# Performance work log

Measured on AMD Instinct MI355X. Metric: run time of the kernel, lower is better.

The kernel has to match this reference:

```python
import jax, jax.numpy as jnp
import numpy as np

B, N_PER_GRAPH = 16, 512          # uniform graphs -> to_dense_batch is a reshape
N_TOKENS = B * N_PER_GRAPH
M = 32                            # neighbors per node
D_MODEL, D_EDGE, H = 256, 128, 8


def _layernorm(x, g, b, eps=1e-5):
    m = jnp.mean(x, axis=-1, keepdims=True)
    v = jnp.mean((x - m) ** 2, axis=-1, keepdims=True)
    return (x - m) * jax.lax.rsqrt(v + eps) * g + b


def _frame_ops():
    # 2^3 = 8 sign-flip operations, matches FrameAveraging.create_ops
    d = jnp.array([-1.0, 1.0], dtype=jnp.float32)
    g = jnp.meshgrid(d, d, d, indexing='ij')
    return jnp.stack(g, axis=-1).reshape(8, 3)


def _forward(token_embs, geo_feats, edge_feats, neighbor_indices, neighbor_masks,
             ln_qkv_g, ln_qkv_b, W_qkv, b_qkv, ln_e_g, ln_e_b, W_qkv_e, b_qkv_e,
             w_attn, w_edge, W_gate, b_gate, W_fc1, b_fc1, ln_h_g, ln_h_b,
             W_fc2, b_fc2, W_fa, b_fa):
    n = token_embs.shape[0]
    d_head = D_MODEL // H
    de_head = D_EDGE // H
    # qkv transformation
    qkv = _layernorm(token_embs, ln_qkv_g, ln_qkv_b) @ W_qkv + b_qkv
    q, k, v = [a.reshape(n, H, d_head) for a in jnp.split(qkv, 3, axis=-1)]
    qkve = _layernorm(edge_feats, ln_e_g, ln_e_b) @ W_qkv_e + b_qkv_e
    qe, ve = [a.reshape(n, M, H, de_head) for a in jnp.split(qkve, 2, axis=-1)]
    gate = jax.nn.sigmoid(token_embs @ W_gate + b_gate)            # [n,1]
    # GAT-style MLP attention over gathered neighbors
    message = q[:, None] + k[neighbor_indices]                     # [n,M,H,d]
    attn = jnp.einsum('nmhd,d->nmh', message, w_attn) \
         + jnp.einsum('nmhe,e->nmh', qe, w_edge)
    attn = jnp.where(neighbor_masks[..., None], attn, -1e9)
    attn = jax.nn.softmax(jnp.transpose(attn, (0, 2, 1)), axis=-1)  # [n,H,M]
    # context aggregation
    v_n = v[neighbor_indices]                                      # [n,M,H,d]
    scalar_ctx = jnp.einsum('nhm,nmhd->nhd', attn, v_n).reshape(n, -1)
    edge_ctx = jnp.einsum('nhm,nmhd->nhd', attn, ve).reshape(n, -1)
    hcat = jnp.concatenate([scalar_ctx, edge_ctx], axis=-1)
    hmid = _layernorm(jax.nn.gelu(hcat @ W_fc1 + b_fc1, approximate=False), ln_h_g, ln_h_b)
    scalar_out = hmid @ W_fc2 + b_fc2 + token_embs
    # geometric branch with frame averaging (n_heads > 1 path)
    Xb = geo_feats.reshape(B, N_PER_GRAPH, 3)                      # dense batch, full mask
    center = Xb.mean(axis=1)                                       # [B,3]
    Xc = Xb - center[:, None]
    C = jax.lax.stop_gradient(jnp.einsum('bni,bnj->bij', Xc, Xc))  # backward=False -> detach
    _, V = jnp.linalg.eigh(C)                                      # symmetric, UPLO irrelevant
    ops = _frame_ops()
    F_ops = jax.lax.stop_gradient(ops[None, :, None, :] * V[:, None])  # [B,8,3,3]
    h_fr = jnp.einsum('bpj,boji->bopi', Xc, F_ops)                 # [B,8,N,3]
    geo_f = jnp.transpose(h_fr, (1, 0, 2, 3)).reshape(8, n, 3)     # frame-major, node order b*N+p
    geo_neigh = geo_f[:, neighbor_indices]                         # [8,n,M,3]
    geo_ctx = jnp.einsum('nhm,fnmd->fnhd', attn, geo_neigh)        # [8,n,H,3]
    agg = jax.nn.silu(jnp.einsum('fnhd,h->fnd', geo_ctx, W_fa) + b_fa)  # W_frame_agg
    geo_b = jnp.transpose(agg, (1, 0, 2)).reshape(B, N_PER_GRAPH, 8, 3)
    geo_b = jnp.transpose(geo_b, (0, 2, 1, 3))                     # [B,8,N,3]
    inv = jnp.einsum('boij,bopj->bopi', F_ops, geo_b).mean(axis=1) + center[:, None]
    geo_context = inv.reshape(n, 3)
    geo_out = geo_context * gate + geo_feats * (1.0 - gate)
    return scalar_out, geo_out


def setup_inputs() -> dict:
    key = jax.random.key(0)
    ks = jax.random.split(key, 16)
    r = lambda k, shape, s=0.02: (jax.random.normal(k, shape) * s).astype(jnp.float32)
    token_embs = jax.random.normal(ks[0], (N_TOKENS, D_MODEL), dtype=jnp.float32)
    geo_feats = jax.random.normal(ks[1], (N_TOKENS, 3), dtype=jnp.float32)
    edge_feats = jax.random.normal(ks[2], (N_TOKENS, M, D_EDGE), dtype=jnp.float32)
    base = (jnp.arange(N_TOKENS) // N_PER_GRAPH) * N_PER_GRAPH
    neighbor_indices = base[:, None] + jax.random.randint(ks[3], (N_TOKENS, M), 0, N_PER_GRAPH)
    batch_idx = jnp.arange(N_TOKENS) // N_PER_GRAPH
    neighbor_masks = jax.random.uniform(ks[4], (N_TOKENS, M)) < 0.9
    d_head, de_head = D_MODEL // H, D_EDGE // H
    return dict(
        token_embs=token_embs, geo_feats=geo_feats, edge_feats=edge_feats,
        neighbor_indices=neighbor_indices, batch_idx=batch_idx, neighbor_masks=neighbor_masks,
        ln_qkv_g=jnp.ones(D_MODEL), ln_qkv_b=jnp.zeros(D_MODEL),
        W_qkv=r(ks[5], (D_MODEL, 3 * D_MODEL)), b_qkv=jnp.zeros(3 * D_MODEL),
        ln_e_g=jnp.ones(D_EDGE), ln_e_b=jnp.zeros(D_EDGE),
        W_qkv_e=r(ks[6], (D_EDGE, 2 * D_EDGE)), b_qkv_e=jnp.zeros(2 * D_EDGE),
        w_attn=r(ks[7], (d_head,), 0.1), w_edge=r(ks[8], (de_head,), 0.1),
        W_gate=jnp.zeros((D_MODEL, 1)), b_gate=jnp.ones((1,)),   # _init_params
        W_fc1=r(ks[9], (D_MODEL + D_EDGE, D_MODEL)), b_fc1=jnp.zeros(D_MODEL),
        ln_h_g=jnp.ones(D_MODEL), ln_h_b=jnp.zeros(D_MODEL),
        W_fc2=r(ks[10], (D_MODEL, D_MODEL)), b_fc2=jnp.zeros(D_MODEL),
        W_fa=r(ks[11], (H,), 0.3), b_fa=jnp.zeros((1,)),
    )


def reference(token_embs, geo_feats, edge_feats, neighbor_indices, batch_idx, neighbor_masks,
              ln_qkv_g, ln_qkv_b, W_qkv, b_qkv, ln_e_g, ln_e_b, W_qkv_e, b_qkv_e,
              w_attn, w_edge, W_gate, b_gate, W_fc1, b_fc1, ln_h_g, ln_h_b,
              W_fc2, b_fc2, W_fa, b_fa):
    # batch_idx is uniform (arange // N_PER_GRAPH); dense batching handled by reshape
    return _forward(token_embs, geo_feats, edge_feats, neighbor_indices, neighbor_masks,
                    ln_qkv_g, ln_qkv_b, W_qkv, b_qkv, ln_e_g, ln_e_b, W_qkv_e, b_qkv_e,
                    w_attn, w_edge, W_gate, b_gate, W_fc1, b_fc1, ln_h_g, ln_h_b,
                    W_fc2, b_fc2, W_fa, b_fa)
```

## Files before the change

### kernel.cpp

```cpp
#include <hip/hip_runtime.h>
#include <math.h>

#define NTOK 8192
#define NPG  512
#define MNEI 32
#define DM   256
#define DE   128
#define NH   8

#define OFF_WCAT  0u
#define OFF_BCAT  69632u
#define OFF_WEF   69904u
#define OFF_BEF   70928u
#define OFF_FLAG  70936u
#define OFF_QA    70944u
#define OFF_KA    136480u
#define OFF_GATE  202016u
#define OFF_VW    210208u
#define OFF_PROJ  2307360u
#define OFF_VMAT  2331936u
#define OFF_CEN   2332080u
#define OFF_HCAT  2332128u

#define OUT_GEO_OFF 2097152

__device__ __forceinline__ void fma16(const float* row, float w, float* acc) {
    const float4* r4 = (const float4*)row;
    float4 a0 = r4[0], a1 = r4[1], a2 = r4[2], a3 = r4[3];
    acc[0]  += a0.x*w; acc[1]  += a0.y*w; acc[2]  += a0.z*w; acc[3]  += a0.w*w;
    acc[4]  += a1.x*w; acc[5]  += a1.y*w; acc[6]  += a1.z*w; acc[7]  += a1.w*w;
    acc[8]  += a2.x*w; acc[9]  += a2.y*w; acc[10] += a2.z*w; acc[11] += a2.w*w;
    acc[12] += a3.x*w; acc[13] += a3.y*w; acc[14] += a3.z*w; acc[15] += a3.w*w;
}

__global__ __launch_bounds__(256) void k_fold(
    const float* __restrict__ Wqkv, const float* __restrict__ bqkv,
    const float* __restrict__ Wqkve, const float* __restrict__ bqkve,
    const float* __restrict__ w_attn, const float* __restrict__ w_edge,
    const int* __restrict__ maskp, float* __restrict__ ws)
{
    int t = threadIdx.x;
    if (blockIdx.x == 0) {
        __shared__ int sbad, sflt;
        if (t == 0) { sbad = 0; sflt = 0; }
        __syncthreads();
        int bad = 0, flt = 0;
        for (int i = 0; i < 256; i++) {
            unsigned int w = (unsigned int)maskp[t*256 + i];
            if (w > 1u) bad = 1;
            if (w == 0x3F800000u) flt = 1;
        }
        if (bad) atomicOr(&sbad, 1);
        if (flt) atomicOr(&sflt, 1);
        __syncthreads();
        if (t == 0) {
            int f = sflt ? 2 : (sbad ? 1 : 0);
            ((int*)(ws + OFF_FLAG))[0] = f;
        }
        return;
    }
    int gid = (blockIdx.x - 1) * 256 + t;
    if (gid < 69632) {
        int r = gid / 272, c = gid % 272;
        float val;
        if (c < 16) {
            int h = c & 7; int off = (c < 8) ? 0 : 256;
            float s = 0.f;
            for (int d = 0; d < 32; d++) s += Wqkv[r*768 + off + h*32 + d] * w_attn[d];
            val = s;
        } else {
            val = Wqkv[r*768 + 512 + (c - 16)];
        }
        ws[OFF_WCAT + gid] = val;
    } else if (gid < 69632 + 272) {
        int c = gid - 69632;
        float val;
        if (c < 16) {
            int h = c & 7; int off = (c < 8) ? 0 : 256;
            float s = 0.f;
            for (int d = 0; d < 32; d++) s += bqkv[off + h*32 + d] * w_attn[d];
            val = s;
        } else {
            val = bqkv[512 + (c - 16)];
        }
        ws[OFF_BCAT + c] = val;
    } else if (gid < 69904 + 1024) {
        int i = gid - 69904;
        int h = i >> 7, r = i & 127;
        float s = 0.f;
        for (int e = 0; e < 16; e++) s += Wqkve[r*256 + h*16 + e] * w_edge[e];
        ws[OFF_WEF + i] = s;
    } else if (gid < 70928 + 8) {
        int h = gid - 70928;
        float s = 0.f;
        for (int e = 0; e < 16; e++) s += bqkve[h*16 + e] * w_edge[e];
        ws[OFF_BEF + h] = s;
    }
}

__global__ __launch_bounds__(320) void k_tokprep(
    const float* __restrict__ tok, const float* __restrict__ ln_g,
    const float* __restrict__ ln_b, const float* __restrict__ Wgate,
    const float* __restrict__ bgate, float* __restrict__ ws)
{
    __shared__ __align__(16) float sln[256 * 20];
    int t = threadIdx.x;
    int tok0 = blockIdx.x * 16;

    for (int i = t; i < 16 * 256; i += 320) {
        int tt = i >> 8, k = i & 255;
        sln[k*20 + tt] = tok[(size_t)(tok0 + tt) * 256 + k];
    }
    __syncthreads();

    int wave = t >> 6, lane = t & 63;
    if (wave < 4) {
        for (int rr = 0; rr < 4; rr++) {
            int tt = wave * 4 + rr;
            float s = 0.f, gdot = 0.f;
            float xs[4];
            for (int i = 0; i < 4; i++) {
                int k = lane + 64 * i;
                float x = sln[k*20 + tt];
                xs[i] = x; s += x; gdot += x * Wgate[k];
            }
            for (int m = 32; m >= 1; m >>= 1) { s += __shfl_xor(s, m, 64); gdot += __shfl_xor(gdot, m, 64); }
            float mu = s * (1.0f / 256.0f);
            float vs = 0.f;
            for (int i = 0; i < 4; i++) { float d = xs[i] - mu; vs += d * d; }
            for (int m = 32; m >= 1; m >>= 1) vs += __shfl_xor(vs, m, 64);
            float rinv = rsqrtf(vs * (1.0f / 256.0f) + 1e-5f);
            for (int i = 0; i < 4; i++) {
                int k = lane + 64 * i;
                sln[k*20 + tt] = (xs[i] - mu) * rinv * ln_g[k] + ln_b[k];
            }
            if (lane == 0) ws[OFF_GATE + tok0 + tt] = 1.0f / (1.0f + expf(-(gdot + bgate[0])));
        }
    }
    __syncthreads();

    if (t < 272) {
        const float* Wc = ws + OFF_WCAT;
        float acc[16];
        #pragma unroll
        for (int i = 0; i < 16; i++) acc[i] = 0.f;
        #pragma unroll 4
        for (int k = 0; k < 256; k++) {
            float w = Wc[k*272 + t];
            fma16(&sln[k*20], w, acc);
        }
        float b = ws[OFF_BCAT + t];
        for (int tt = 0; tt < 16; tt++) {
            float val = acc[tt] + b;
            int n = tok0 + tt;
            if (t < 8)       ws[OFF_QA + n*8 + t] = val;
            else if (t < 16) ws[OFF_KA + n*8 + (t - 8)] = val;
            else             ws[OFF_VW + (size_t)n*256 + (t - 16)] = val;
        }
    }
}

__global__ __launch_bounds__(256) void k_geo(const float* __restrict__ geo, float* __restrict__ ws)
{
    __shared__ float sred[4 * 9];
    __shared__ float sres[9];
    __shared__ float sV[9];
    int t = threadIdx.x, g = blockIdx.x;
    int wave = t >> 6, lane = t & 63;
    const float* gp = geo + (size_t)g * NPG * 3;

    float x0[2], y0[2], z0[2];
    float sx = 0.f, sy = 0.f, sz = 0.f;
    for (int i = 0; i < 2; i++) {
        int p = t + 256 * i;
        x0[i] = gp[p*3 + 0]; y0[i] = gp[p*3 + 1]; z0[i] = gp[p*3 + 2];
        sx += x0[i]; sy += y0[i]; sz += z0[i];
    }
    {
        float vals[3] = {sx, sy, sz};
        for (int q = 0; q < 3; q++) {
            float v = vals[q];
            for (int m = 32; m >= 1; m >>= 1) v += __shfl_xor(v, m, 64);
            if (lane == 0) sred[wave*9 + q] = v;
        }
    }
    __syncthreads();
    if (t < 3) {
        float s = 0.f;
        for (int w = 0; w < 4; w++) s += sred[w*9 + t];
        sres[t] = s * (1.0f / 512.0f);
    }
    __syncthreads();
    float cx = sres[0], cy = sres[1], cz = sres[2];

    float c6[6] = {0.f, 0.f, 0.f, 0.f, 0.f, 0.f};
    for (int i = 0; i < 2; i++) {
        float dx = x0[i] - cx, dy = y0[i] - cy, dz = z0[i] - cz;
        c6[0] += dx*dx; c6[1] += dx*dy; c6[2] += dx*dz;
        c6[3] += dy*dy; c6[4] += dy*dz; c6[5] += dz*dz;
    }
    for (int q = 0; q < 6; q++) {
        float v = c6[q];
        for (int m = 32; m >= 1; m >>= 1) v += __shfl_xor(v, m, 64);
        if (lane == 0) sred[wave*9 + q] = v;
    }
    __syncthreads();
    if (t < 6) {
        float s = 0.f;
        for (int w = 0; w < 4; w++) s += sred[w*9 + t];
        sres[t] = s;
    }
    __syncthreads();

    if (t == 0) {
        double a[3][3];
        a[0][0] = sres[0]; a[0][1] = a[1][0] = sres[1]; a[0][2] = a[2][0] = sres[2];
        a[1][1] = sres[3]; a[1][2] = a[2][1] = sres[4]; a[2][2] = sres[5];
        double v[3][3] = {{1,0,0},{0,1,0},{0,0,1}};
        const int ps[3] = {0, 0, 1}, qs[3] = {1, 2, 2};
        for (int sweep = 0; sweep < 30; sweep++) {
            for (int pi = 0; pi < 3; pi++) {
                int p = ps[pi], q = qs[pi];
                double apq = a[p][q];
                if (fabs(apq) < 1e-300) continue;
                double theta = (a[q][q] - a[p][p]) / (2.0 * apq);
                double tt = ((theta >= 0.0) ? 1.0 : -1.0) / (fabs(theta) + sqrt(theta*theta + 1.0));
                double c = 1.0 / sqrt(tt*tt + 1.0), s = tt * c;
                int k = 3 - p - q;
                double app = a[p][p], aqq = a[q][q], akp = a[k][p], akq = a[k][q];
                a[p][p] = app - tt * apq;
                a[q][q] = aqq + tt * apq;
                a[p][q] = 0.0; a[q][p] = 0.0;
                a[k][p] = c*akp - s*akq; a[p][k] = a[k][p];
                a[k][q] = s*akp + c*akq; a[q][k] = a[k][q];
                for (int kk = 0; kk < 3; kk++) {
                    double vp = v[kk][p], vq = v[kk][q];
                    v[kk][p] = c*vp - s*vq;
                    v[kk][q] = s*vp + c*vq;
                }
            }
        }
        for (int r = 0; r < 3; r++)
            for (int c2 = 0; c2 < 3; c2++) {
                float fv = (float)v[r][c2];
                sV[r*3 + c2] = fv;
                ws[OFF_VMAT + g*9 + r*3 + c2] = fv;
            }
        ws[OFF_CEN + g*3 + 0] = cx;
        ws[OFF_CEN + g*3 + 1] = cy;
        ws[OFF_CEN + g*3 + 2] = cz;
    }
    __syncthreads();

    for (int i = 0; i < 2; i++) {
        int p = t + 256 * i;
        float dx = x0[i] - cx, dy = y0[i] - cy, dz = z0[i] - cz;
        for (int c = 0; c < 3; c++) {
            float pr = dx * sV[0*3 + c] + dy * sV[1*3 + c] + dz * sV[2*3 + c];
            ws[OFF_PROJ + (size_t)(g*NPG + p)*3 + c] = pr;
        }
    }
}

__global__ __launch_bounds__(256) void k_attn(
    const float* __restrict__ edge, const int* __restrict__ nbr,
    const void* __restrict__ maskp,
    const float* __restrict__ lneg, const float* __restrict__ lneb,
    const float* __restrict__ bqkve, const float* __restrict__ Wqkve,
    const float* __restrict__ Wfa, const float* __restrict__ bfa,
    const float* __restrict__ geo, float* __restrict__ ws, float* __restrict__ out)
{
    __shared__ __align__(16) float se[32 * 132];
    __shared__ __align__(16) float swe[8 * 132];
    __shared__ __align__(16) float sew[8 * 132];
    __shared__ float slog[264];
    __shared__ float sattn[264];
    __shared__ int   snbr[32];
    __shared__ int   smask[32];
    __shared__ float swm[32];
    __shared__ float sqa[8], sbef[8];
    __shared__ float sge[128], sbe[128];
    __shared__ float sg3[3];

    int t = threadIdx.x;
    int n = blockIdx.x;
    int g = n >> 9;
    int flag = ((const int*)(ws + OFF_FLAG))[0];

    if (t < 32) {
        snbr[t] = nbr[n*32 + t];
        int mv;
        if (flag == 1)      mv = (int)((const unsigned char*)maskp)[n*32 + t];
        else if (flag == 2) mv = (((const float*)maskp)[n*32 + t] != 0.0f) ? 1 : 0;
        else                mv = ((const int*)maskp)[n*32 + t];
        smask[t] = mv;
    }
    if (t < 8) { sqa[t] = ws[OFF_QA + n*8 + t]; sbef[t] = ws[OFF_BEF + t]; }
    if (t >= 32 && t < 160) { sge[t - 32] = lneg[t - 32]; sbe[t - 32] = lneb[t - 32]; }
    {
        const float* wef = ws + OFF_WEF;
        for (int i = 0; i < 4; i++) {
            int idx = t*4 + i;
            int h = idx >> 7, r = idx & 127;
            swe[h*132 + r] = wef[idx];
        }
    }
    {
        const float4* ep = (const float4*)(edge + (size_t)n * 4096);
        for (int j = 0; j < 4; j++) {
            int l = j*1024 + t*4;
            float4 v4 = ep[l >> 2];
            int m = l >> 7, r = l & 127;
            *(float4*)&se[m*132 + r] = v4;
        }
    }
    __syncthreads();

    {
        int m = t >> 3, sub = t & 7;
        int base = m*132 + sub*16;
        float4 x0 = *(float4*)&se[base + 0];
        float4 x1 = *(float4*)&se[base + 4];
        float4 x2 = *(float4*)&se[base + 8];
        float4 x3 = *(float4*)&se[base + 12];
        float s = x0.x+x0.y+x0.z+x0.w + x1.x+x1.y+x1.z+x1.w
                + x2.x+x2.y+x2.z+x2.w + x3.x+x3.y+x3.z+x3.w;
        for (int mm = 4; mm >= 1; mm >>= 1) s += __shfl_xor(s, mm, 8);
        float mu = s * (1.0f / 128.0f);
        float vs = (x0.x-mu)*(x0.x-mu) + (x0.y-mu)*(x0.y-mu) + (x0.z-mu)*(x0.z-mu) + (x0.w-mu)*(x0.w-mu)
                 + (x1.x-mu)*(x1.x-mu) + (x1.y-mu)*(x1.y-mu) + (x1.z-mu)*(x1.z-mu) + (x1.w-mu)*(x1.w-mu)
                 + (x2.x-mu)*(x2.x-mu) + (x2.y-mu)*(x2.y-mu) + (x2.z-mu)*(x2.z-mu) + (x2.w-mu)*(x2.w-mu)
                 + (x3.x-mu)*(x3.x-mu) + (x3.y-mu)*(x3.y-mu) + (x3.z-mu)*(x3.z-mu) + (x3.w-mu)*(x3.w-mu);
        for (int mm = 4; mm >= 1; mm >>= 1) vs += __shfl_xor(vs, mm, 8);
        float rinv = rsqrtf(vs * (1.0f / 128.0f) + 1e-5f);
        int r0 = sub * 16;
        x0.x = (x0.x-mu)*rinv*sge[r0+0]  + sbe[r0+0];  x0.y = (x0.y-mu)*rinv*sge[r0+1]  + sbe[r0+1];
        x0.z = (x0.z-mu)*rinv*sge[r0+2]  + sbe[r0+2];  x0.w = (x0.w-mu)*rinv*sge[r0+3]  + sbe[r0+3];
        x1.x = (x1.x-mu)*rinv*sge[r0+4]  + sbe[r0+4];  x1.y = (x1.y-mu)*rinv*sge[r0+5]  + sbe[r0+5];
        x1.z = (x1.z-mu)*rinv*sge[r0+6]  + sbe[r0+6];  x1.w = (x1.w-mu)*rinv*sge[r0+7]  + sbe[r0+7];
        x2.x = (x2.x-mu)*rinv*sge[r0+8]  + sbe[r0+8];  x2.y = (x2.y-mu)*rinv*sge[r0+9]  + sbe[r0+9];
        x2.z = (x2.z-mu)*rinv*sge[r0+10] + sbe[r0+10]; x2.w = (x2.w-mu)*rinv*sge[r0+11] + sbe[r0+11];
        x3.x = (x3.x-mu)*rinv*sge[r0+12] + sbe[r0+12]; x3.y = (x3.y-mu)*rinv*sge[r0+13] + sbe[r0+13];
        x3.z = (x3.z-mu)*rinv*sge[r0+14] + sbe[r0+14]; x3.w = (x3.w-mu)*rinv*sge[r0+15] + sbe[r0+15];
        *(float4*)&se[base + 0]  = x0;
        *(float4*)&se[base + 4]  = x1;
        *(float4*)&se[base + 8]  = x2;
        *(float4*)&se[base + 12] = x3;
    }
    __syncthreads();

    {
        int m = t >> 3, h = t & 7;
        float acc = sbef[h];
        #pragma unroll 8
        for (int r = 0; r < 128; r += 4) {
            float4 e4 = *(float4*)&se[m*132 + r];
            float4 w4 = *(float4*)&swe[h*132 + r];
            acc += e4.x*w4.x + e4.y*w4.y + e4.z*w4.z + e4.w*w4.w;
        }
        float lg = sqa[h] + ws[OFF_KA + snbr[m]*8 + h] + acc;
        if (!smask[m]) lg = -1e9f;
        slog[h*33 + m] = lg;
    }
    __syncthreads();

    {
        int h = t >> 5, m = t & 31;
        float x = slog[h*33 + m];
        float mx = x;
        for (int mm = 16; mm >= 1; mm >>= 1) mx = fmaxf(mx, __shfl_xor(mx, mm, 32));
        float e = expf(x - mx);
        float sum = e;
        for (int mm = 16; mm >= 1; mm >>= 1) sum += __shfl_xor(sum, mm, 32);
        sattn[h*33 + m] = e / sum;
    }
    __syncthreads();

    {
        int h = t >> 5;
        float acc = 0.f;
        const float* vw = ws + OFF_VW;
        #pragma unroll 4
        for (int m = 0; m < 32; m++) {
            int row = snbr[m];
            acc += sattn[h*33 + m] * vw[(size_t)row*256 + t];
        }
        ws[OFF_HCAT + (size_t)n*384 + t] = acc;
    }

    {
        int h = t >> 5, r0 = t & 31;
        for (int i = 0; i < 4; i++) {
            int r = r0 + 32 * i;
            float acc = 0.f;
            #pragma unroll 8
            for (int m = 0; m < 32; m++) acc += sattn[h*33 + m] * se[m*132 + r];
            sew[h*132 + r] = acc;
        }
    }
    if (t < 32) {
        float acc = 0.f;
        for (int h = 0; h < 8; h++) acc += Wfa[h] * sattn[h*33 + t];
        swm[t] = acc;
    }
    __syncthreads();

    if (t < 128) {
        int h = t >> 4;
        float acc = bqkve[128 + t];
        #pragma unroll 8
        for (int r = 0; r < 128; r++) acc += sew[h*132 + r] * Wqkve[r*256 + 128 + t];
        ws[OFF_HCAT + (size_t)n*384 + 256 + t] = acc;
    }

    if (t < 3) {
        float sd = 0.f;
        for (int m = 0; m < 32; m++) sd += swm[m] * ws[OFF_PROJ + (size_t)snbr[m]*3 + t];
        float bb = bfa[0];
        float p1 = sd + bb, p2 = -sd + bb;
        float s1v = p1 / (1.0f + expf(-p1));
        float s2v = p2 / (1.0f + expf(-p2));
        sg3[t] = 0.5f * (s1v - s2v);
    }
    __syncthreads();
    if (t < 3) {
        const float* Vm = ws + OFF_VMAT + g*9;
        float gc = Vm[t*3+0]*sg3[0] + Vm[t*3+1]*sg3[1] + Vm[t*3+2]*sg3[2] + ws[OFF_CEN + g*3 + t];
        float gt = ws[OFF_GATE + n];
        out[OUT_GEO_OFF + (size_t)n*3 + t] = gc * gt + geo[(size_t)n*3 + t] * (1.0f - gt);
    }
}

__global__ __launch_bounds__(256) void k_mlp(
    const float* __restrict__ tok, const float* __restrict__ Wfc1,
    const float* __restrict__ bfc1, const float* __restrict__ lnhg,
    const float* __restrict__ lnhb, const float* __restrict__ Wfc2,
    const float* __restrict__ bfc2, const float* __restrict__ ws,
    float* __restrict__ out)
{
    __shared__ __align__(16) float s1[384 * 20];
    int t = threadIdx.x;
    int tok0 = blockIdx.x * 16;
    const float* hc = ws + OFF_HCAT;

    for (int i = 0; i < 24; i++) {
        int idx = i*256 + t;
        int tt = idx / 384;
        int k  = idx - tt*384;
        s1[k*20 + tt] = hc[(size_t)tok0*384 + idx];
    }
    __syncthreads();

    float h[16];
    {
        float acc[16];
        #pragma unroll
        for (int i = 0; i < 16; i++) acc[i] = 0.f;
        #pragma unroll 4
        for (int k = 0; k < 384; k++) {
            float w = Wfc1[k*256 + t];
            fma16(&s1[k*20], w, acc);
        }
        float b = bfc1[t];
        for (int tt = 0; tt < 16; tt++) {
            float x = acc[tt] + b;
            h[tt] = 0.5f * x * (1.0f + erff(x * 0.70710678118654752f));
        }
    }
    __syncthreads();
    for (int tt = 0; tt < 16; tt++) s1[t*20 + tt] = h[tt];
    __syncthreads();

    {
        int wave = t >> 6, lane = t & 63;
        for (int rr = 0; rr < 4; rr++) {
            int tt = wave * 4 + rr;
            float s = 0.f;
            float xs[4];
            for (int i = 0; i < 4; i++) {
                int k = lane + 64 * i;
                xs[i] = s1[k*20 + tt];
                s += xs[i];
            }
            for (int m = 32; m >= 1; m >>= 1) s += __shfl_xor(s, m, 64);
            float mu = s * (1.0f / 256.0f);
            float vs = 0.f;
            for (int i = 0; i < 4; i++) { float d = xs[i] - mu; vs += d * d; }
            for (int m = 32; m >= 1; m >>= 1) vs += __shfl_xor(vs, m, 64);
            float rinv = rsqrtf(vs * (1.0f / 256.0f) + 1e-5f);
            for (int i = 0; i < 4; i++) {
                int k = lane + 64 * i;
                s1[k*20 + tt] = (xs[i] - mu) * rinv * lnhg[k] + lnhb[k];
            }
        }
    }
    __syncthreads();

    {
        float acc[16];
        #pragma unroll
        for (int i = 0; i < 16; i++) acc[i] = 0.f;
        #pragma unroll 4
        for (int k = 0; k < 256; k++) {
            float w = Wfc2[k*256 + t];
            fma16(&s1[k*20], w, acc);
        }
        float b = bfc2[t];
        for (int tt = 0; tt < 16; tt++) {
            size_t o = (size_t)(tok0 + tt) * 256 + t;
            out[o] = acc[tt] + b + tok[o];
        }
    }
}

extern "C" void kernel_launch(void* const* d_in, const int* in_sizes, int n_in,
                              void* d_out, int out_size, void* d_ws, size_t ws_size,
                              hipStream_t stream) {
    (void)in_sizes; (void)n_in; (void)out_size; (void)ws_size;
    const float* tok   = (const float*)d_in[0];
    const float* geo   = (const float*)d_in[1];
    const float* edge  = (const float*)d_in[2];
    const int*   nbr   = (const int*)d_in[3];
    const void*  maskp = d_in[5];
    const float* ln_qkv_g = (const float*)d_in[6];
    const float* ln_qkv_b = (const float*)d_in[7];
    const float* Wqkv  = (const float*)d_in[8];
    const float* bqkv  = (const float*)d_in[9];
    const float* ln_e_g = (const float*)d_in[10];
    const float* ln_e_b = (const float*)d_in[11];
    const float* Wqkve = (const float*)d_in[12];
    const float* bqkve = (const float*)d_in[13];
    const float* w_attn = (const float*)d_in[14];
    const float* w_edge = (const float*)d_in[15];
    const float* Wgate = (const float*)d_in[16];
    const float* bgate = (const float*)d_in[17];
    const float* Wfc1  = (const float*)d_in[18];
    const float* bfc1  = (const float*)d_in[19];
    const float* lnhg  = (const float*)d_in[20];
    const float* lnhb  = (const float*)d_in[21];
    const float* Wfc2  = (const float*)d_in[22];
    const float* bfc2  = (const float*)d_in[23];
    const float* Wfa   = (const float*)d_in[24];
    const float* bfa   = (const float*)d_in[25];
    float* ws  = (float*)d_ws;
    float* out = (float*)d_out;

    k_fold<<<dim3(279), dim3(256), 0, stream>>>(Wqkv, bqkv, Wqkve, bqkve, w_attn, w_edge,
                                                (const int*)maskp, ws);
    k_tokprep<<<dim3(512), dim3(320), 0, stream>>>(tok, ln_qkv_g, ln_qkv_b, Wgate, bgate, ws);
    k_geo<<<dim3(16), dim3(256), 0, stream>>>(geo, ws);
    k_attn<<<dim3(8192), dim3(256), 0, stream>>>(edge, nbr, maskp, ln_e_g, ln_e_b, bqkve,
                                                 Wqkve, Wfa, bfa, geo, ws, out);
    k_mlp<<<dim3(512), dim3(256), 0, stream>>>(tok, Wfc1, bfc1, lnhg, lnhb, Wfc2, bfc2, ws, out);
}
```

Baseline: 466.0 us.

## Retile token GEMMs as 4x4 register blocks and restructure attention edge projection

The tokprep and MLP GEMMs move from one-column, sixteen-token accumulation to 4x4 register tiles with float4 weight loads and float4 stores. The MLP layernorm becomes a single-pass shuffle reduction that uses the sum of squares. In attention, the edge-context projection is split across all 256 threads in two halves, the frame-averaging dot products are parallelised, and one shared buffer is removed. Also included are a coalesced mask scan, fewer Jacobi sweeps, and a deeper unroll. The single-pass variance is slightly less numerically stable, and cutting Jacobi to 10 sweeps may risk eigenvector convergence.

New measurement: 441.6 us. 1.06x faster.

```diff
diff --git a/kernel.cpp b/kernel.cpp
--- a/kernel.cpp
+++ b/kernel.cpp
@@ -24,13 +24,11 @@
 
 #define OUT_GEO_OFF 2097152
 
-__device__ __forceinline__ void fma16(const float* row, float w, float* acc) {
-    const float4* r4 = (const float4*)row;
-    float4 a0 = r4[0], a1 = r4[1], a2 = r4[2], a3 = r4[3];
-    acc[0]  += a0.x*w; acc[1]  += a0.y*w; acc[2]  += a0.z*w; acc[3]  += a0.w*w;
-    acc[4]  += a1.x*w; acc[5]  += a1.y*w; acc[6]  += a1.z*w; acc[7]  += a1.w*w;
-    acc[8]  += a2.x*w; acc[9]  += a2.y*w; acc[10] += a2.z*w; acc[11] += a2.w*w;
-    acc[12] += a3.x*w; acc[13] += a3.y*w; acc[14] += a3.z*w; acc[15] += a3.w*w;
+__device__ __forceinline__ void fma4x4(const float4 a, const float4 w, float4* acc) {
+    acc[0].x += a.x*w.x; acc[0].y += a.x*w.y; acc[0].z += a.x*w.z; acc[0].w += a.x*w.w;
+    acc[1].x += a.y*w.x; acc[1].y += a.y*w.y; acc[1].z += a.y*w.z; acc[1].w += a.y*w.w;
+    acc[2].x += a.z*w.x; acc[2].y += a.z*w.y; acc[2].z += a.z*w.z; acc[2].w += a.z*w.w;
+    acc[3].x += a.w*w.x; acc[3].y += a.w*w.y; acc[3].z += a.w*w.z; acc[3].w += a.w*w.w;
 }
 
 __global__ __launch_bounds__(256) void k_fold(
@@ -46,7 +44,7 @@
         __syncthreads();
         int bad = 0, flt = 0;
         for (int i = 0; i < 256; i++) {
-            unsigned int w = (unsigned int)maskp[t*256 + i];
+            unsigned int w = (unsigned int)maskp[i*256 + t];
             if (w > 1u) bad = 1;
             if (w == 0x3F800000u) flt = 1;
         }
@@ -107,8 +105,8 @@
     int t = threadIdx.x;
     int tok0 = blockIdx.x * 16;
 
-    for (int i = t; i < 16 * 256; i += 320) {
-        int tt = i >> 8, k = i & 255;
+    for (int idx = t; idx < 4096; idx += 320) {
+        int tt = idx >> 8, k = idx & 255;
         sln[k*20 + tt] = tok[(size_t)(tok0 + tt) * 256 + k];
     }
     __syncthreads();
@@ -119,43 +117,52 @@
             int tt = wave * 4 + rr;
             float s = 0.f, gdot = 0.f;
             float xs[4];
-            for (int i = 0; i < 4; i++) {
-                int k = lane + 64 * i;
+            for (int q = 0; q < 4; q++) {
+                int k = lane + 64*q;
                 float x = sln[k*20 + tt];
-                xs[i] = x; s += x; gdot += x * Wgate[k];
-            }
-            for (int m = 32; m >= 1; m >>= 1) { s += __shfl_xor(s, m, 64); gdot += __shfl_xor(gdot, m, 64); }
-            float mu = s * (1.0f / 256.0f);
+                xs[q] = x; s += x; gdot += x * Wgate[k];
+            }
+            for (int m = 32; m >= 1; m >>= 1) { s += __shfl_xor(s,m,64); gdot += __shfl_xor(gdot,m,64); }
+            float mu = s * (1.0f/256.0f);
             float vs = 0.f;
-            for (int i = 0; i < 4; i++) { float d = xs[i] - mu; vs += d * d; }
-            for (int m = 32; m >= 1; m >>= 1) vs += __shfl_xor(vs, m, 64);
-            float rinv = rsqrtf(vs * (1.0f / 256.0f) + 1e-5f);
-            for (int i = 0; i < 4; i++) {
-                int k = lane + 64 * i;
-                sln[k*20 + tt] = (xs[i] - mu) * rinv * ln_g[k] + ln_b[k];
-            }
-            if (lane == 0) ws[OFF_GATE + tok0 + tt] = 1.0f / (1.0f + expf(-(gdot + bgate[0])));
+            for (int q = 0; q < 4; q++) { float d = xs[q]-mu; vs += d*d; }
+            for (int m = 32; m >= 1; m >>= 1) vs += __shfl_xor(vs,m,64);
+            float rinv = rsqrtf(vs*(1.0f/256.0f)+1e-5f);
+            for (int q = 0; q < 4; q++) {
+                int k = lane + 64*q;
+                sln[k*20 + tt] = (xs[q]-mu)*rinv*ln_g[k] + ln_b[k];
+            }
+            if (lane == 0) ws[OFF_GATE + tok0 + tt] = 1.0f/(1.0f+expf(-(gdot + bgate[0])));
         }
     }
     __syncthreads();
 
     if (t < 272) {
-        const float* Wc = ws + OFF_WCAT;
-        float acc[16];
-        #pragma unroll
-        for (int i = 0; i < 16; i++) acc[i] = 0.f;
+        int i = t / 68, j = t - i*68;
+        const float* Wc = ws + OFF_WCAT + 4*j;
+        float4 acc[4];
+        acc[0] = acc[1] = acc[2] = acc[3] = make_float4(0.f,0.f,0.f,0.f);
         #pragma unroll 4
         for (int k = 0; k < 256; k++) {
-            float w = Wc[k*272 + t];
-            fma16(&sln[k*20], w, acc);
-        }
-        float b = ws[OFF_BCAT + t];
-        for (int tt = 0; tt < 16; tt++) {
-            float val = acc[tt] + b;
-            int n = tok0 + tt;
-            if (t < 8)       ws[OFF_QA + n*8 + t] = val;
-            else if (t < 16) ws[OFF_KA + n*8 + (t - 8)] = val;
-            else             ws[OFF_VW + (size_t)n*256 + (t - 16)] = val;
+            float4 a4 = *(const float4*)&sln[k*20 + 4*i];
+            float4 w4 = *(const float4*)&Wc[(size_t)k*272];
+            fma4x4(a4, w4, acc);
+        }
+        float4 b4 = *(const float4*)&ws[OFF_BCAT + 4*j];
+        for (int ti = 0; ti < 4; ti++) {
+            int n = tok0 + 4*i + ti;
+            float4 v = acc[ti];
+            v.x += b4.x; v.y += b4.y; v.z += b4.z; v.w += b4.w;
+            if (j >= 4) {
+                *(float4*)&ws[OFF_VW + (size_t)n*256 + (4*j - 16)] = v;
+            } else {
+                float vv[4] = {v.x, v.y, v.z, v.w};
+                for (int c = 0; c < 4; c++) {
+                    int col = 4*j + c;
+                    if (col < 8) ws[OFF_QA + n*8 + col] = vv[c];
+                    else         ws[OFF_KA + n*8 + (col-8)] = vv[c];
+                }
+            }
         }
     }
 }
@@ -218,7 +225,7 @@
         a[1][1] = sres[3]; a[1][2] = a[2][1] = sres[4]; a[2][2] = sres[5];
         double v[3][3] = {{1,0,0},{0,1,0},{0,0,1}};
         const int ps[3] = {0, 0, 1}, qs[3] = {1, 2, 2};
-        for (int sweep = 0; sweep < 30; sweep++) {
+        for (int sweep = 0; sweep < 10; sweep++) {
             for (int pi = 0; pi < 3; pi++) {
                 int p = ps[pi], q = qs[pi];
                 double apq = a[p][q];
@@ -272,7 +279,6 @@
 {
     __shared__ __align__(16) float se[32 * 132];
     __shared__ __align__(16) float swe[8 * 132];
-    __shared__ __align__(16) float sew[8 * 132];
     __shared__ float slog[264];
     __shared__ float sattn[264];
     __shared__ int   snbr[32];
@@ -280,7 +286,7 @@
     __shared__ float swm[32];
     __shared__ float sqa[8], sbef[8];
     __shared__ float sge[128], sbe[128];
-    __shared__ float sg3[3];
+    __shared__ float sg3[4];
 
     int t = threadIdx.x;
     int n = blockIdx.x;
@@ -380,23 +386,23 @@
         int h = t >> 5;
         float acc = 0.f;
         const float* vw = ws + OFF_VW;
-        #pragma unroll 4
+        #pragma unroll 8
         for (int m = 0; m < 32; m++) {
             int row = snbr[m];
             acc += sattn[h*33 + m] * vw[(size_t)row*256 + t];
         }
         ws[OFF_HCAT + (size_t)n*384 + t] = acc;
     }
-
-    {
-        int h = t >> 5, r0 = t & 31;
-        for (int i = 0; i < 4; i++) {
-            int r = r0 + 32 * i;
-            float acc = 0.f;
-            #pragma unroll 8
-            for (int m = 0; m < 32; m++) acc += sattn[h*33 + m] * se[m*132 + r];
-            sew[h*132 + r] = acc;
-        }
+    {
+        int h = t >> 5, rq = (t & 31) * 4;
+        float4 acc = make_float4(0.f,0.f,0.f,0.f);
+        #pragma unroll 8
+        for (int m = 0; m < 32; m++) {
+            float a = sattn[h*33 + m];
+            float4 e4 = *(float4*)&se[m*132 + rq];
+            acc.x += a*e4.x; acc.y += a*e4.y; acc.z += a*e4.z; acc.w += a*e4.w;
+        }
+        *(float4*)&swe[h*132 + rq] = acc;
     }
     if (t < 32) {
         float acc = 0.f;
@@ -405,17 +411,33 @@
     }
     __syncthreads();
 
+    float accEC;
+    {
+        int col = t & 127, half = t >> 7;
+        int h2 = col >> 4;
+        int rbase = half * 64;
+        const float* wq = Wqkve + 128 + col;
+        float a0 = 0.f;
+        #pragma unroll 8
+        for (int r = 0; r < 64; r++)
+            a0 += swe[h2*132 + rbase + r] * wq[(size_t)(rbase + r)*256];
+        accEC = a0;
+        if (half) slog[col] = a0;
+    }
+    if (t >= 128 && t < 224) {
+        int idx = t - 128;
+        int m = idx / 3, c = idx - m*3;
+        slog[128 + idx] = swm[m] * ws[OFF_PROJ + (size_t)snbr[m]*3 + c];
+    }
+    __syncthreads();
+
     if (t < 128) {
-        int h = t >> 4;
-        float acc = bqkve[128 + t];
-        #pragma unroll 8
-        for (int r = 0; r < 128; r++) acc += sew[h*132 + r] * Wqkve[r*256 + 128 + t];
-        ws[OFF_HCAT + (size_t)n*384 + 256 + t] = acc;
-    }
-
+        float tot = accEC + slog[t] + bqkve[128 + t];
+        ws[OFF_HCAT + (size_t)n*384 + 256 + t] = tot;
+    }
     if (t < 3) {
         float sd = 0.f;
-        for (int m = 0; m < 32; m++) sd += swm[m] * ws[OFF_PROJ + (size_t)snbr[m]*3 + t];
+        for (int m = 0; m < 32; m++) sd += slog[128 + m*3 + t];
         float bb = bfa[0];
         float p1 = sd + bb, p2 = -sd + bb;
         float s1v = p1 / (1.0f + expf(-p1));
@@ -423,6 +445,7 @@
         sg3[t] = 0.5f * (s1v - s2v);
     }
     __syncthreads();
+
     if (t < 3) {
         const float* Vm = ws + OFF_VMAT + g*9;
         float gc = Vm[t*3+0]*sg3[0] + Vm[t*3+1]*sg3[1] + Vm[t*3+2]*sg3[2] + ws[OFF_CEN + g*3 + t];
@@ -438,77 +461,93 @@
     const float* __restrict__ bfc2, const float* __restrict__ ws,
     float* __restrict__ out)
 {
-    __shared__ __align__(16) float s1[384 * 20];
+    __shared__ __align__(16) float A[384 * 20];
     int t = threadIdx.x;
     int tok0 = blockIdx.x * 16;
+    int i = t >> 6, j = t & 63;
     const float* hc = ws + OFF_HCAT;
 
-    for (int i = 0; i < 24; i++) {
-        int idx = i*256 + t;
+    for (int it = 0; it < 24; it++) {
+        int idx = it*256 + t;
         int tt = idx / 384;
         int k  = idx - tt*384;
-        s1[k*20 + tt] = hc[(size_t)tok0*384 + idx];
-    }
-    __syncthreads();
-
-    float h[16];
-    {
-        float acc[16];
-        #pragma unroll
-        for (int i = 0; i < 16; i++) acc[i] = 0.f;
+        A[k*20 + tt] = hc[(size_t)tok0*384 + idx];
+    }
+    __syncthreads();
+
+    float4 acc1[4];
+    acc1[0] = acc1[1] = acc1[2] = acc1[3] = make_float4(0.f,0.f,0.f,0.f);
+    {
+        const float* wp = Wfc1 + 4*j;
         #pragma unroll 4
         for (int k = 0; k < 384; k++) {
-            float w = Wfc1[k*256 + t];
-            fma16(&s1[k*20], w, acc);
-        }
-        float b = bfc1[t];
-        for (int tt = 0; tt < 16; tt++) {
-            float x = acc[tt] + b;
-            h[tt] = 0.5f * x * (1.0f + erff(x * 0.70710678118654752f));
-        }
-    }
-    __syncthreads();
-    for (int tt = 0; tt < 16; tt++) s1[t*20 + tt] = h[tt];
-    __syncthreads();
-
-    {
-        int wave = t >> 6, lane = t & 63;
-        for (int rr = 0; rr < 4; rr++) {
-            int tt = wave * 4 + rr;
-            float s = 0.f;
-            float xs[4];
-            for (int i = 0; i < 4; i++) {
-                int k = lane + 64 * i;
-                xs[i] = s1[k*20 + tt];
-                s += xs[i];
-            }
-            for (int m = 32; m >= 1; m >>= 1) s += __shfl_xor(s, m, 64);
-            float mu = s * (1.0f / 256.0f);
-            float vs = 0.f;
-            for (int i = 0; i < 4; i++) { float d = xs[i] - mu; vs += d * d; }
-            for (int m = 32; m >= 1; m >>= 1) vs += __shfl_xor(vs, m, 64);
-            float rinv = rsqrtf(vs * (1.0f / 256.0f) + 1e-5f);
-            for (int i = 0; i < 4; i++) {
-                int k = lane + 64 * i;
-                s1[k*20 + tt] = (xs[i] - mu) * rinv * lnhg[k] + lnhb[k];
-            }
-        }
-    }
-    __syncthreads();
-
-    {
-        float acc[16];
-        #pragma unroll
-        for (int i = 0; i < 16; i++) acc[i] = 0.f;
+            float4 a4 = *(const float4*)&A[k*20 + 4*i];
+            float4 w4 = *(const float4*)&wp[(size_t)k*256];
+            fma4x4(a4, w4, acc1);
+        }
+    }
+    float h[4][4];
+    {
+        float4 b4 = *(const float4*)&bfc1[4*j];
+        for (int ti = 0; ti < 4; ti++) {
+            float xv[4] = {acc1[ti].x + b4.x, acc1[ti].y + b4.y, acc1[ti].z + b4.z, acc1[ti].w + b4.w};
+            for (int c = 0; c < 4; c++) {
+                float x = xv[c];
+                h[ti][c] = 0.5f * x * (1.0f + erff(x * 0.70710678118654752f));
+            }
+        }
+    }
+    __syncthreads();
+
+    {
+        float s[4], q[4];
+        for (int ti = 0; ti < 4; ti++) {
+            s[ti] = h[ti][0] + h[ti][1] + h[ti][2] + h[ti][3];
+            q[ti] = h[ti][0]*h[ti][0] + h[ti][1]*h[ti][1] + h[ti][2]*h[ti][2] + h[ti][3]*h[ti][3];
+        }
+        for (int m = 32; m >= 1; m >>= 1)
+            for (int ti = 0; ti < 4; ti++) {
+                s[ti] += __shfl_xor(s[ti], m, 64);
+                q[ti] += __shfl_xor(q[ti], m, 64);
+            }
+        float4 g4 = *(const float4*)&lnhg[4*j];
+        float4 b4 = *(const float4*)&lnhb[4*j];
+        float gg[4] = {g4.x, g4.y, g4.z, g4.w};
+        float bb[4] = {b4.x, b4.y, b4.z, b4.w};
+        for (int ti = 0; ti < 4; ti++) {
+            float mu = s[ti] * (1.0f/256.0f);
+            float var = q[ti] * (1.0f/256.0f) - mu*mu;
+            float rinv = rsqrtf(var + 1e-5f);
+            for (int c = 0; c < 4; c++) {
+                float hn = (h[ti][c] - mu) * rinv * gg[c] + bb[c];
+                A[(4*j + c)*20 + 4*i + ti] = hn;
+            }
+        }
+    }
+    __syncthreads();
+
+    float4 acc2[4];
+    acc2[0] = acc2[1] = acc2[2] = acc2[3] = make_float4(0.f,0.f,0.f,0.f);
+    {
+        const float* wp = Wfc2 + 4*j;
         #pragma unroll 4
         for (int k = 0; k < 256; k++) {
-            float w = Wfc2[k*256 + t];
-            fma16(&s1[k*20], w, acc);
-        }
-        float b = bfc2[t];
-        for (int tt = 0; tt < 16; tt++) {
-            size_t o = (size_t)(tok0 + tt) * 256 + t;
-            out[o] = acc[tt] + b + tok[o];
+            float4 a4 = *(const float4*)&A[k*20 + 4*i];
+            float4 w4 = *(const float4*)&wp[(size_t)k*256];
+            fma4x4(a4, w4, acc2);
+        }
+    }
+    {
+        float4 b4 = *(const float4*)&bfc2[4*j];
+        for (int ti = 0; ti < 4; ti++) {
+            size_t o = (size_t)(tok0 + 4*i + ti) * 256 + 4*j;
+            float4 r4 = *(const float4*)&tok[o];
+            float4 v;
+            v.x = acc2[ti].x + b4.x + r4.x;
+            v.y = acc2[ti].y + b4.y + r4.y;
+            v.z = acc2[ti].z + b4.z + r4.z;
+            v.w = acc2[ti].w + b4.w + r4.w;
+            *(float4*)&out[o] = v;
         }
     }
 }
```
